# Kernel tuning notes

Measured on AMD Instinct MI355X. Metric: run time of the kernel, lower is better.

## Reference

```python
import jax, jax.numpy as jnp
import numpy as np

EPS = 1e-12  # torch F.normalize eps

def _l2norm(x):
    # matches torch.nn.functional.normalize(x, dim=-1): x / max(||x||, eps)
    n = jnp.sqrt(jnp.sum(x * x, axis=-1, keepdims=True))
    return x / jnp.maximum(n, EPS)

def setup_inputs() -> dict:
    key = jax.random.key(0)
    k1, k2, k3 = jax.random.split(key, 3)
    N, D, H, C = 4096, 16384, 256, 28
    return {
        "features": jax.random.normal(k1, (N, H), dtype=jnp.float32),
        "ex_features": jax.random.normal(k2, (D, H), dtype=jnp.float32),
        "ex_class_reps": jax.random.normal(k3, (D, C), dtype=jnp.float32),
        "p_factor": 3,
    }

def reference(features, ex_features, ex_class_reps, p_factor):
    # cosine similarity: [N, D]
    s = _l2norm(features) @ _l2norm(ex_features).T
    # power-law activation preserving sign
    a = jnp.sign(s) * jnp.abs(s) ** p_factor
    intensity = a.sum(axis=1)           # [N]
    echo = a @ ex_class_reps            # [N, C]
    return (echo, intensity)
```

## Files before the change

kernel.cpp:

```cpp
#include <hip/hip_runtime.h>
#include <cstdint>

#define HDIM 256
#define MT   256
#define BDW  16
#define SPLITS 32
#define RPB  16

typedef short bf16x8 __attribute__((ext_vector_type(8)));
typedef short bf16x4 __attribute__((ext_vector_type(4)));
typedef float f32x4  __attribute__((ext_vector_type(4)));

typedef const __attribute__((address_space(1))) short as1_short;
typedef __attribute__((address_space(3))) short as3_short;

static __device__ __forceinline__ short f2bf(float x) {
    union { float f; uint32_t u; } v; v.f = x;
    uint32_t u = v.u;
    uint32_t r = (u + 0x7fffu + ((u >> 16) & 1u)) >> 16;
    return (short)r;
}

__global__ __launch_bounds__(256) void prep_kernel(const float* __restrict__ fsrc,
                                                   const float* __restrict__ esrc,
                                                   const float* __restrict__ reps,
                                                   short* __restrict__ dst,
                                                   short* __restrict__ rt,
                                                   int N, int rows_total,
                                                   int D, int C, int nb_nrm) {
    __shared__ float lds[128][29];
    const int tid = threadIdx.x;
    if ((int)blockIdx.x < nb_nrm) {
        int wv = tid >> 6;
        int lane = tid & 63;
        int row0 = blockIdx.x * RPB + wv * 4;
        #pragma unroll
        for (int rr = 0; rr < 4; ++rr) {
            int row = row0 + rr;
            if (row >= rows_total) continue;
            const float* src = (row < N) ? (fsrc + (size_t)row * HDIM)
                                         : (esrc + (size_t)(row - N) * HDIM);
            const float4 v = *(const float4*)(src + lane * 4);
            float ss = v.x * v.x + v.y * v.y + v.z * v.z + v.w * v.w;
            #pragma unroll
            for (int m = 1; m < 64; m <<= 1) ss += __shfl_xor(ss, m, 64);
            float scale = 1.0f / fmaxf(sqrtf(ss), 1e-12f);
            short4 o;
            o.x = f2bf(v.x * scale); o.y = f2bf(v.y * scale);
            o.z = f2bf(v.z * scale); o.w = f2bf(v.w * scale);
            int chunk = (lane >> 1) ^ (row & 7);
            *(short4*)(dst + (size_t)row * HDIM + chunk * 8 + (lane & 1) * 4) = o;
        }
    } else {
        const int bx = blockIdx.x - nb_nrm;
        const int d0 = bx * 128;
        const int total = 128 * C;
        const float* src = reps + (size_t)d0 * C;
        for (int i = tid; i < total; i += 256)
            lds[i / C][i % C] = src[i];
        __syncthreads();
        const int c = tid >> 3;
        const int dsub = (tid & 7) * 16;
        short* dstp = rt + (size_t)c * D + d0 + dsub;
        #pragma unroll
        for (int j0 = 0; j0 < 16; j0 += 4) {
            short4 o;
            float v0, v1, v2, v3;
            if (c < C) {
                v0 = lds[dsub + j0 + 0][c]; v1 = lds[dsub + j0 + 1][c];
                v2 = lds[dsub + j0 + 2][c]; v3 = lds[dsub + j0 + 3][c];
            } else {
                float f = (c == C) ? 1.0f : 0.0f;
                v0 = v1 = v2 = v3 = f;
            }
            o.x = f2bf(v0); o.y = f2bf(v1); o.z = f2bf(v2); o.w = f2bf(v3);
            *(short4*)(dstp + j0) = o;
        }
    }
}

__global__ __launch_bounds__(256, 2) void fused_kernel(const short* __restrict__ Fn,
                                                       const short* __restrict__ En,
                                                       const short* __restrict__ Rt,
                                                       const int* __restrict__ pptr,
                                                       float* __restrict__ partial,
                                                       int N, int D, int C, int Dchunk) {
    __shared__ __align__(16) short lds_en[4][2][BDW * HDIM];

    const int tid  = threadIdx.x;
    const int lane = tid & 63;
    const int wv   = tid >> 6;
    const int q    = lane >> 4;
    const int l    = lane & 15;
    const int p    = pptr[0];

    const int Mbase = blockIdx.y * MT;
    const int dbase = blockIdx.x * Dchunk;

    const f32x4 zf = {0.0f, 0.0f, 0.0f, 0.0f};

    bf16x8 afrag[4][8];
    #pragma unroll
    for (int fn = 0; fn < 4; ++fn) {
        const short* rowp = Fn + (size_t)(Mbase + wv * 64 + fn * 16 + l) * HDIM;
        #pragma unroll
        for (int ks = 0; ks < 8; ++ks)
            afrag[fn][ks] = *(const bf16x8*)(rowp + (((ks * 4 + q) ^ (l & 7)) << 3));
    }

    f32x4 echo_acc[4][2];
    #pragma unroll
    for (int fn = 0; fn < 4; ++fn) { echo_acc[fn][0] = zf; echo_acc[fn][1] = zf; }

    const int nwin = Dchunk / BDW;

    #define STAGE_W(buf_, it_)                                                      \
        {                                                                           \
            const short* gbase = En + (size_t)(dbase + (it_) * BDW) * HDIM + lane * 8;\
            as3_short* lbase = (as3_short*)(&lds_en[wv][buf_][0]);                  \
            _Pragma("unroll")                                                       \
            for (int i = 0; i < 8; ++i) {                                           \
                __builtin_amdgcn_global_load_lds((as1_short*)(gbase + i * 512),     \
                                                 lbase + i * 512, 16, 0, 0);        \
            }                                                                       \
        }

    const short* rtp = Rt + (size_t)l * D + q * 4;

    STAGE_W(0, 0)
    STAGE_W(1, 1)

    for (int it = 0; it < nwin; ++it) {
        const int buf = it & 1;

        if (it < nwin - 1) {
            asm volatile("s_waitcnt vmcnt(8)" ::: "memory");
        } else {
            asm volatile("s_waitcnt vmcnt(0)" ::: "memory");
        }
        __builtin_amdgcn_sched_barrier(0);

        const int d0 = dbase + it * BDW;

        f32x4 sT[4];
        #pragma unroll
        for (int fn = 0; fn < 4; ++fn) sT[fn] = zf;
        #pragma unroll
        for (int ks = 0; ks < 8; ++ks) {
            const int slot = (ks * 4 + q) ^ (l & 7);
            bf16x8 ef = *(const bf16x8*)(&lds_en[wv][buf][l * HDIM + slot * 8]);
            #pragma unroll
            for (int fn = 0; fn < 4; ++fn)
                sT[fn] = __builtin_amdgcn_mfma_f32_16x16x32_bf16(ef, afrag[fn][ks], sT[fn], 0, 0, 0);
        }

        bf16x4 rt0 = *(const bf16x4*)(rtp + d0);
        bf16x4 rt1 = *(const bf16x4*)(rtp + (size_t)16 * D + d0);

        asm volatile("s_waitcnt lgkmcnt(0)" ::: "memory");
        __builtin_amdgcn_sched_barrier(0);
        if (it + 2 < nwin) STAGE_W(buf, it + 2)

        bf16x4 pfrag[4];
        #pragma unroll
        for (int fn = 0; fn < 4; ++fn) {
            bf16x4 pf;
            #pragma unroll
            for (int r = 0; r < 4; ++r) {
                float sv = sT[fn][r];
                float a;
                if (p == 3)      a = sv * sv * sv;
                else if (p == 1) a = sv;
                else if (p == 2) a = sv * fabsf(sv);
                else             a = copysignf(powf(fabsf(sv), (float)p), sv);
                pf[r] = f2bf(a);
            }
            pfrag[fn] = pf;
        }

        #pragma unroll
        for (int fn = 0; fn < 4; ++fn) {
            echo_acc[fn][0] = __builtin_amdgcn_mfma_f32_16x16x16bf16_1k(rt0, pfrag[fn], echo_acc[fn][0], 0, 0, 0);
            echo_acc[fn][1] = __builtin_amdgcn_mfma_f32_16x16x16bf16_1k(rt1, pfrag[fn], echo_acc[fn][1], 0, 0, 0);
        }
    }

    #pragma unroll
    for (int fn = 0; fn < 4; ++fn) {
        const int grow = Mbase + wv * 64 + fn * 16 + l;
        float* rowp = partial + ((size_t)blockIdx.x * N + grow) * 32 + q * 4;
        *(f32x4*)(rowp)      = echo_acc[fn][0];
        *(f32x4*)(rowp + 16) = echo_acc[fn][1];
    }

    #undef STAGE_W
}

__global__ __launch_bounds__(256) void reduce_kernel(const float* __restrict__ partial,
                                                     float* __restrict__ echo,
                                                     float* __restrict__ inten,
                                                     int N, int splits, int C) {
    int t = blockIdx.x * 256 + threadIdx.x;
    int row = t >> 5, c = t & 31;
    if (row >= N || c > C) return;
    float s = 0.0f;
    for (int k = 0; k < splits; ++k)
        s += partial[((size_t)k * N + (size_t)row) * 32 + c];
    if (c < C) echo[(size_t)row * C + c] = s;
    else       inten[row] = s;
}

extern "C" void kernel_launch(void* const* d_in, const int* in_sizes, int n_in,
                              void* d_out, int out_size, void* d_ws, size_t ws_size,
                              hipStream_t stream) {
    const int N = in_sizes[0] / HDIM;
    const int D = in_sizes[1] / HDIM;
    const int C = in_sizes[2] / D;

    const float* feat = (const float*)d_in[0];
    const float* exf  = (const float*)d_in[1];
    const float* reps = (const float*)d_in[2];
    const int*   p    = (const int*)d_in[3];

    short* Fn = (short*)d_ws;
    short* En = Fn + (size_t)N * HDIM;
    short* Rt = En + (size_t)D * HDIM;
    float* partial = (float*)(Rt + (size_t)32 * D);

    float* echo  = (float*)d_out;
    float* inten = echo + (size_t)N * C;

    const int nb_nrm = (N + D + RPB - 1) / RPB;
    hipLaunchKernelGGL(prep_kernel, dim3(nb_nrm + D / 128), dim3(256), 0, stream,
                       feat, exf, reps, Fn, Rt, N, N + D, D, C, nb_nrm);

    const int Dchunk = D / SPLITS;
    hipLaunchKernelGGL(fused_kernel, dim3(SPLITS, N / MT), dim3(256), 0, stream,
                       Fn, En, Rt, p, partial, N, D, C, Dchunk);

    hipLaunchKernelGGL(reduce_kernel, dim3(N * 32 / 256), dim3(256), 0, stream,
                       partial, echo, inten, N, SPLITS, C);
}
```

Baseline: 141.2 us.

## Share staged ex_feature windows across waves through block-wide LDS batches

Before, each of the four waves staged its own copy of the same 16-row ex_feature window into private LDS, so every window was fetched from global memory four times. Now each wave stages a different window of a 4-window batch into shared LDS, double-buffered across batches with a __syncthreads per batch. All four waves then consume all four windows, and the class-rep fragments for the whole batch are loaded up front. This cuts redundant global/L2 traffic by four, at the cost of a block-wide barrier each batch and coarser prefetch granularity.

```diff
diff --git a/kernel.cpp b/kernel.cpp
--- a/kernel.cpp
+++ b/kernel.cpp
@@ -4,6 +4,7 @@
 #define HDIM 256
 #define MT   256
 #define BDW  16
+#define BWIN 4
 #define SPLITS 32
 #define RPB  16
 
@@ -85,7 +86,7 @@
                                                        const int* __restrict__ pptr,
                                                        float* __restrict__ partial,
                                                        int N, int D, int C, int Dchunk) {
-    __shared__ __align__(16) short lds_en[4][2][BDW * HDIM];
+    __shared__ __align__(16) short lds_en[2][BWIN][BDW * HDIM];
 
     const int tid  = threadIdx.x;
     const int lane = tid & 63;
@@ -112,12 +113,13 @@
     #pragma unroll
     for (int fn = 0; fn < 4; ++fn) { echo_acc[fn][0] = zf; echo_acc[fn][1] = zf; }
 
-    const int nwin = Dchunk / BDW;
-
-    #define STAGE_W(buf_, it_)                                                      \
+    const int nbatch = Dchunk / (BDW * BWIN);
+
+    #define STAGE_BATCH(buf_, b_)                                                   \
         {                                                                           \
-            const short* gbase = En + (size_t)(dbase + (it_) * BDW) * HDIM + lane * 8;\
-            as3_short* lbase = (as3_short*)(&lds_en[wv][buf_][0]);                  \
+            const short* gbase = En + (size_t)(dbase + ((b_) * BWIN + wv) * BDW) * HDIM \
+                               + lane * 8;                                          \
+            as3_short* lbase = (as3_short*)(&lds_en[buf_][wv][0]);                  \
             _Pragma("unroll")                                                       \
             for (int i = 0; i < 8; ++i) {                                           \
                 __builtin_amdgcn_global_load_lds((as1_short*)(gbase + i * 512),     \
@@ -127,61 +129,60 @@
 
     const short* rtp = Rt + (size_t)l * D + q * 4;
 
-    STAGE_W(0, 0)
-    STAGE_W(1, 1)
-
-    for (int it = 0; it < nwin; ++it) {
-        const int buf = it & 1;
-
-        if (it < nwin - 1) {
-            asm volatile("s_waitcnt vmcnt(8)" ::: "memory");
-        } else {
-            asm volatile("s_waitcnt vmcnt(0)" ::: "memory");
+    STAGE_BATCH(0, 0)
+
+    for (int b = 0; b < nbatch; ++b) {
+        const int cur = b & 1;
+
+        __syncthreads();
+
+        bf16x4 rt_all[BWIN][2];
+        #pragma unroll
+        for (int w = 0; w < BWIN; ++w) {
+            const int d0 = dbase + (b * BWIN + w) * BDW;
+            rt_all[w][0] = *(const bf16x4*)(rtp + d0);
+            rt_all[w][1] = *(const bf16x4*)(rtp + (size_t)16 * D + d0);
         }
         __builtin_amdgcn_sched_barrier(0);
 
-        const int d0 = dbase + it * BDW;
-
-        f32x4 sT[4];
-        #pragma unroll
-        for (int fn = 0; fn < 4; ++fn) sT[fn] = zf;
-        #pragma unroll
-        for (int ks = 0; ks < 8; ++ks) {
-            const int slot = (ks * 4 + q) ^ (l & 7);
-            bf16x8 ef = *(const bf16x8*)(&lds_en[wv][buf][l * HDIM + slot * 8]);
-            #pragma unroll
-            for (int fn = 0; fn < 4; ++fn)
-                sT[fn] = __builtin_amdgcn_mfma_f32_16x16x32_bf16(ef, afrag[fn][ks], sT[fn], 0, 0, 0);
-        }
-
-        bf16x4 rt0 = *(const bf16x4*)(rtp + d0);
-        bf16x4 rt1 = *(const bf16x4*)(rtp + (size_t)16 * D + d0);
-
-        asm volatile("s_waitcnt lgkmcnt(0)" ::: "memory");
-        __builtin_amdgcn_sched_barrier(0);
-        if (it + 2 < nwin) STAGE_W(buf, it + 2)
-
-        bf16x4 pfrag[4];
-        #pragma unroll
-        for (int fn = 0; fn < 4; ++fn) {
-            bf16x4 pf;
-            #pragma unroll
-            for (int r = 0; r < 4; ++r) {
-                float sv = sT[fn][r];
-                float a;
-                if (p == 3)      a = sv * sv * sv;
-                else if (p == 1) a = sv;
-                else if (p == 2) a = sv * fabsf(sv);
-                else             a = copysignf(powf(fabsf(sv), (float)p), sv);
-                pf[r] = f2bf(a);
-            }
-            pfrag[fn] = pf;
-        }
-
-        #pragma unroll
-        for (int fn = 0; fn < 4; ++fn) {
-            echo_acc[fn][0] = __builtin_amdgcn_mfma_f32_16x16x16bf16_1k(rt0, pfrag[fn], echo_acc[fn][0], 0, 0, 0);
-            echo_acc[fn][1] = __builtin_amdgcn_mfma_f32_16x16x16bf16_1k(rt1, pfrag[fn], echo_acc[fn][1], 0, 0, 0);
+        if (b + 1 < nbatch) STAGE_BATCH(cur ^ 1, b + 1)
+
+        #pragma unroll
+        for (int w = 0; w < BWIN; ++w) {
+            f32x4 sT[4];
+            #pragma unroll
+            for (int fn = 0; fn < 4; ++fn) sT[fn] = zf;
+            #pragma unroll
+            for (int ks = 0; ks < 8; ++ks) {
+                const int slot = (ks * 4 + q) ^ (l & 7);
+                bf16x8 ef = *(const bf16x8*)(&lds_en[cur][w][l * HDIM + slot * 8]);
+                #pragma unroll
+                for (int fn = 0; fn < 4; ++fn)
+                    sT[fn] = __builtin_amdgcn_mfma_f32_16x16x32_bf16(ef, afrag[fn][ks], sT[fn], 0, 0, 0);
+            }
+
+            bf16x4 pfrag[4];
+            #pragma unroll
+            for (int fn = 0; fn < 4; ++fn) {
+                bf16x4 pf;
+                #pragma unroll
+                for (int r = 0; r < 4; ++r) {
+                    float sv = sT[fn][r];
+                    float a;
+                    if (p == 3)      a = sv * sv * sv;
+                    else if (p == 1) a = sv;
+                    else if (p == 2) a = sv * fabsf(sv);
+                    else             a = copysignf(powf(fabsf(sv), (float)p), sv);
+                    pf[r] = f2bf(a);
+                }
+                pfrag[fn] = pf;
+            }
+
+            #pragma unroll
+            for (int fn = 0; fn < 4; ++fn) {
+                echo_acc[fn][0] = __builtin_amdgcn_mfma_f32_16x16x16bf16_1k(rt_all[w][0], pfrag[fn], echo_acc[fn][0], 0, 0, 0);
+                echo_acc[fn][1] = __builtin_amdgcn_mfma_f32_16x16x16bf16_1k(rt_all[w][1], pfrag[fn], echo_acc[fn][1], 0, 0, 0);
+            }
         }
     }
 
@@ -193,7 +194,7 @@
         *(f32x4*)(rowp + 16) = echo_acc[fn][1];
     }
 
-    #undef STAGE_W
+    #undef STAGE_BATCH
 }
 
 __global__ __launch_bounds__(256) void reduce_kernel(const float* __restrict__ partial,
```

Result: no change. 142.9 us (+1.2%).
